# Performance work log

Measured on AMD Instinct MI355X. Metric: run time of the kernel, lower is better.

The kernel has to match this reference:

```python
import jax, jax.numpy as jnp
import numpy as np
import math

CH = 256
HW = 64
B = 4

def setup_inputs() -> dict:
    key = jax.random.key(0)
    ks = jax.random.split(key, 9)
    shp = (B, CH, HW, HW)
    return {
        "query": jax.random.normal(ks[0], shp, dtype=jnp.float32),
        "key":   jax.random.normal(ks[1], shp, dtype=jnp.float32),
        "value": jax.random.normal(ks[2], shp, dtype=jnp.float32),
        "wq": jax.random.normal(ks[3], (CH, CH), dtype=jnp.float32) * (1.0 / math.sqrt(CH)),
        "bq": jax.random.normal(ks[4], (CH,), dtype=jnp.float32) * 0.01,
        "wk": jax.random.normal(ks[5], (CH, CH), dtype=jnp.float32) * (1.0 / math.sqrt(CH)),
        "bk": jax.random.normal(ks[6], (CH,), dtype=jnp.float32) * 0.01,
        "wv": jax.random.normal(ks[7], (CH, CH), dtype=jnp.float32) * (1.0 / math.sqrt(CH)),
        "bv": jax.random.normal(ks[8], (CH,), dtype=jnp.float32) * 0.01,
    }

def _proj_to_tokens(x, w, b):
    # 1x1 conv == channel GEMM; output as (B, N, C) token layout
    Bz, C, H, W = x.shape
    # 'bchw,dc->bhwd' fuses the conv and the permute(0,2,1) after view
    t = jnp.einsum('bchw,dc->bhwd', x, w) + b  # (B,H,W,C)
    return t.reshape(Bz, H * W, C)

def reference(query, key, value, wq, bq, wk, bk, wv, bv):
    Bz, C, H, W = query.shape
    scale = 1.0 / jnp.sqrt(jnp.asarray(C, dtype=query.dtype))
    q = _proj_to_tokens(query, wq, bq)   # (B,N,C)
    k = _proj_to_tokens(key, wk, bk)     # (B,N,C)
    v = _proj_to_tokens(value, wv, bv)   # (B,N,C)
    attn = jnp.einsum('bnc,bmc->bnm', q, k) * scale  # (B,N,N)
    attn = jax.nn.softmax(attn, axis=-1)
    out = jnp.einsum('bnm,bmc->bnc', attn, v)        # (B,N,C)
    # permute back to (B,C,H,W)
    return out.transpose(0, 2, 1).reshape(Bz, C, H, W)
```

## Files before the change

### kernel.cpp

```cpp
#include <hip/hip_runtime.h>

typedef __attribute__((ext_vector_type(8))) short bf16x8;
typedef __attribute__((ext_vector_type(4))) float f32x4;
typedef __attribute__((ext_vector_type(4))) unsigned int u32x4;
typedef __attribute__((ext_vector_type(2))) unsigned int u32x2;

#define NTOK 4096
#define CHD 256
#define QSCALE 0.09016844005556022f
#define KB 32
#define NIT 32
#define RESCALE_THR 8.0f

typedef unsigned int __attribute__((address_space(1))) gu32;
typedef unsigned int __attribute__((address_space(3))) lu32;
#define GLOAD(g, s) __builtin_amdgcn_global_load_lds((const gu32*)(const void*)(g), (lu32*)(void*)(s), 16, 0, 0)

__device__ __forceinline__ unsigned short f2bf(float x) {
    unsigned int u = __builtin_bit_cast(unsigned int, x);
    return (unsigned short)((u + 0x7FFFu + ((u >> 16) & 1u)) >> 16);
}
__device__ __forceinline__ float bf2f(unsigned short u) {
    return __builtin_bit_cast(float, (unsigned int)u << 16);
}
__device__ __forceinline__ f32x4 mfma16(bf16x8 a, bf16x8 b, f32x4 c) {
    return __builtin_amdgcn_mfma_f32_16x16x32_bf16(a, b, c, 0, 0, 0);
}
__device__ __forceinline__ float xmax32(float x) {
    x = fmaxf(x, __shfl_xor(x, 16));
    x = fmaxf(x, __shfl_xor(x, 32));
    return x;
}
__device__ __forceinline__ float xsum32(float x) {
    x += __shfl_xor(x, 16);
    x += __shfl_xor(x, 32);
    return x;
}
__device__ __forceinline__ unsigned int cvtpk(float lo, float hi) {
    unsigned int r;
    asm("v_cvt_pk_bf16_f32 %0, %1, %2" : "=v"(r) : "v"(lo), "v"(hi));
    return r;
}

__global__ __launch_bounds__(256) void wconv_kernel(
    const float* __restrict__ wq, const float* __restrict__ wk,
    const float* __restrict__ wv, unsigned short* __restrict__ wbf)
{
    int idx = blockIdx.x * 256 + threadIdx.x;
    int z = idx >> 16;
    const float* src = (z == 0) ? wq : (z == 1) ? wk : wv;
    float s = (z == 0) ? QSCALE : 1.0f;
    wbf[idx] = f2bf(src[idx & 65535] * s);
}

__global__ __launch_bounds__(256) void proj_kernel(
    const float* __restrict__ xq, const float* __restrict__ xk, const float* __restrict__ xv,
    const float* __restrict__ bq, const float* __restrict__ bk, const float* __restrict__ bv,
    const unsigned short* __restrict__ wbf,
    unsigned short* __restrict__ Qo, unsigned short* __restrict__ Ko,
    unsigned short* __restrict__ VTo)
{
    __shared__ __align__(16) unsigned short alds[64 * 264];
    __shared__ __align__(16) unsigned char wlds[16384];
    const int z = blockIdx.y;
    const int b = blockIdx.x >> 6;
    const int n0 = (blockIdx.x & 63) << 6;
    const float* x    = (z == 0) ? xq : (z == 1) ? xk : xv;
    const float* bias = (z == 0) ? bq : (z == 1) ? bk : bv;
    const unsigned short* w = wbf + z * 65536;
    const int t = threadIdx.x;
    const int wv_ = t >> 6, l = t & 63, lr = l & 15, lg = l >> 4;

    #pragma unroll
    for (int it = 0; it < 16; ++it) {
        int idx = it * 256 + t;
        int c = idx >> 4, j4 = idx & 15;
        f32x4 v = *(const f32x4*)(x + (size_t)(b * CHD + c) * NTOK + n0 + j4 * 4);
        #pragma unroll
        for (int i = 0; i < 4; ++i)
            alds[(j4 * 4 + i) * 264 + c] = f2bf(v[i]);
    }
    __syncthreads();

    bf16x8 af[8];
    #pragma unroll
    for (int kk = 0; kk < 8; ++kk)
        af[kk] = *(const bf16x8*)&alds[(wv_ * 16 + lr) * 264 + kk * 32 + lg * 8];

    const float bsc = (z == 0) ? QSCALE : 1.0f;

    for (int dg = 0; dg < 8; ++dg) {
        __syncthreads();
        #pragma unroll
        for (int it = 0; it < 4; ++it) {
            int idx = it * 256 + t;
            int dr = idx >> 5, c16 = idx & 31;
            u32x4 vv = *(const u32x4*)(w + (size_t)(dg * 32 + dr) * CHD + c16 * 8);
            *(u32x4*)(wlds + ((dr * 512 + c16 * 16) ^ ((dr & 7) << 4))) = vv;
        }
        __syncthreads();
        #pragma unroll
        for (int dbi = 0; dbi < 2; ++dbi) {
            int dr = dbi * 16 + lr;
            int d = dg * 32 + dr;
            float bias_v = bias[d] * bsc;
            f32x4 acc = {bias_v, bias_v, bias_v, bias_v};
            #pragma unroll
            for (int kk = 0; kk < 8; ++kk) {
                bf16x8 bf = *(const bf16x8*)(wlds + ((dr * 512 + kk * 64 + lg * 16) ^ ((dr & 7) << 4)));
                acc = mfma16(af[kk], bf, acc);
            }
            if (z < 2) {
                unsigned short* o = (z == 0) ? Qo : Ko;
                #pragma unroll
                for (int r = 0; r < 4; ++r) {
                    int n = n0 + wv_ * 16 + lg * 4 + r;
                    o[(size_t)(b * NTOK + n) * CHD + d] = f2bf(acc[r]);
                }
            } else {
                int n = n0 + wv_ * 16 + lg * 4;
                u32x2 pk;
                pk[0] = (unsigned)f2bf(acc[0]) | ((unsigned)f2bf(acc[1]) << 16);
                pk[1] = (unsigned)f2bf(acc[2]) | ((unsigned)f2bf(acc[3]) << 16);
                *(u32x2*)(VTo + (size_t)(b * CHD + d) * NTOK + n) = pk;
            }
        }
    }
}

__global__ __attribute__((amdgpu_waves_per_eu(2, 2))) __launch_bounds__(512)
void attn_kernel(
    const unsigned short* __restrict__ Qp,
    const unsigned short* __restrict__ Kp,
    const unsigned short* __restrict__ VTp,
    unsigned short* __restrict__ Opart,
    float* __restrict__ Mpart, float* __restrict__ Lpart)
{
    __shared__ __align__(16) char smem[65536];
    const int bid = blockIdx.x;
    const int g = bid & 7, b = g >> 1, hf = g & 1;
    const int j = bid >> 3;
    const int q2 = j >> 4;
    const int n0 = (j & 15) * 256;
    const int part = hf * 2 + q2;
    const int kvbase = hf * 2048 + q2 * 1024;
    const int t = threadIdx.x;
    const int w = t >> 6, l = t & 63, lr = l & 15, lg = l >> 4;

    const char* Kby = (const char*)(Kp + (size_t)b * NTOK * CHD);
    const char* Vby = (const char*)(VTp + (size_t)b * CHD * NTOK);
    const unsigned short* Qb = Qp + (size_t)b * NTOK * CHD;

    bf16x8 qf[2][8];
    #pragma unroll
    for (int nb = 0; nb < 2; ++nb)
        #pragma unroll
        for (int kk = 0; kk < 8; ++kk)
            qf[nb][kk] = *(const bf16x8*)(Qb + (size_t)(n0 + w * 32 + nb * 16 + lr) * CHD + kk * 32 + lg * 8);
    asm volatile("" ::: "memory");

    auto stage = [&](int bsel, int kt2) {
        const char* ks = Kby + (size_t)(kvbase + kt2 * KB) * 512;
        const char* vs = Vby + (size_t)(kvbase + kt2 * KB) * 2;
        char* kd = smem + bsel * 32768 + w * 2048;
        char* vd = smem + bsel * 32768 + 16384 + w * 2048;
        #pragma unroll
        for (int jj = 0; jj < 2; ++jj) {
            int p = w * 2048 + jj * 1024 + l * 16;
            int i = p >> 9, c = p & 511;
            int pi = ((i >> 2) & 3) * 8 + ((i >> 4) & 1) * 4 + (i & 3);
            GLOAD(ks + pi * 512 + (c ^ ((i & 7) << 4)), kd + jj * 1024);
        }
        #pragma unroll
        for (int jj = 0; jj < 2; ++jj) {
            int p = w * 2048 + jj * 1024 + l * 16;
            GLOAD(vs + (p >> 6) * 8192 + (p & 63), vd + jj * 1024);
        }
    };

    stage(0, 0);

    f32x4 o[2][16];
    #pragma unroll
    for (int nb = 0; nb < 2; ++nb)
        #pragma unroll
        for (int db = 0; db < 16; ++db)
            o[nb][db] = (f32x4){0.f, 0.f, 0.f, 0.f};
    float mrow[2] = {-1e30f, -1e30f};
    float lpart[2] = {0.f, 0.f};

    #pragma unroll 1
    for (int kt = 0; kt < NIT; ++kt) {
        const int cur = kt & 1;
        asm volatile("s_waitcnt lgkmcnt(0) vmcnt(0)" ::: "memory");
        __builtin_amdgcn_s_barrier();
        __builtin_amdgcn_sched_barrier(0);
        if (kt + 1 < NIT) stage(cur ^ 1, kt + 1);

        const char* kB = smem + cur * 32768;
        const char* vB = kB + 16384;

        f32x4 s[2][2];
        #pragma unroll
        for (int nb = 0; nb < 2; ++nb)
            #pragma unroll
            for (int cb = 0; cb < 2; ++cb)
                s[nb][cb] = (f32x4){0.f, 0.f, 0.f, 0.f};
        __builtin_amdgcn_s_setprio(1);
        #pragma unroll
        for (int kk = 0; kk < 8; ++kk) {
            #pragma unroll
            for (int cb = 0; cb < 2; ++cb) {
                int row = cb * 16 + lr;
                bf16x8 kf = *(const bf16x8*)(kB + row * 512 + ((kk * 64 + lg * 16) ^ ((row & 7) << 4)));
                s[0][cb] = mfma16(kf, qf[0][kk], s[0][cb]);
                s[1][cb] = mfma16(kf, qf[1][kk], s[1][cb]);
            }
        }
        __builtin_amdgcn_s_setprio(0);

        float pm[2];
        #pragma unroll
        for (int nb = 0; nb < 2; ++nb) {
            float t8 = fmaxf(fmaxf(fmaxf(s[nb][0][0], s[nb][0][1]), fmaxf(s[nb][0][2], s[nb][0][3])),
                             fmaxf(fmaxf(s[nb][1][0], s[nb][1][1]), fmaxf(s[nb][1][2], s[nb][1][3])));
            pm[nb] = xmax32(t8);
        }
        bool grow = (pm[0] > mrow[0] + RESCALE_THR) || (pm[1] > mrow[1] + RESCALE_THR);
        if (__any((int)grow)) {
            #pragma unroll
            for (int nb = 0; nb < 2; ++nb) {
                float mn = fmaxf(mrow[nb], pm[nb]);
                float resc = __builtin_amdgcn_exp2f(mrow[nb] - mn);
                mrow[nb] = mn;
                lpart[nb] *= resc;
                f32x4 r4;
                #pragma unroll
                for (int r = 0; r < 4; ++r)
                    r4[r] = __shfl(resc, lg * 4 + r);
                #pragma unroll
                for (int db = 0; db < 16; ++db)
                    o[nb][db] *= r4;
            }
        }
        bf16x8 pb[2];
        #pragma unroll
        for (int nb = 0; nb < 2; ++nb) {
            float ps = 0.f;
            #pragma unroll
            for (int cb = 0; cb < 2; ++cb)
                #pragma unroll
                for (int r = 0; r < 4; ++r) {
                    float p = __builtin_amdgcn_exp2f(s[nb][cb][r] - mrow[nb]);
                    s[nb][cb][r] = p;
                    ps += p;
                }
            lpart[nb] += ps;
            u32x4 pw;
            pw[0] = cvtpk(s[nb][0][0], s[nb][0][1]);
            pw[1] = cvtpk(s[nb][0][2], s[nb][0][3]);
            pw[2] = cvtpk(s[nb][1][0], s[nb][1][1]);
            pw[3] = cvtpk(s[nb][1][2], s[nb][1][3]);
            pb[nb] = __builtin_bit_cast(bf16x8, pw);
        }

        __builtin_amdgcn_s_setprio(1);
        #pragma unroll
        for (int db = 0; db < 16; ++db) {
            bf16x8 vf = *(const bf16x8*)(vB + (db * 16 + lr) * 64 + lg * 16);
            o[0][db] = mfma16(pb[0], vf, o[0][db]);
            o[1][db] = mfma16(pb[1], vf, o[1][db]);
        }
        __builtin_amdgcn_s_setprio(0);
    }

    float lrow[2];
    #pragma unroll
    for (int nb = 0; nb < 2; ++nb)
        lrow[nb] = xsum32(lpart[nb]);

    unsigned short* Ob = Opart + (size_t)(b * 4 + part) * CHD * NTOK;
    #pragma unroll
    for (int nb = 0; nb < 2; ++nb)
        #pragma unroll
        for (int db = 0; db < 16; ++db) {
            int d = db * 16 + lr;
            int n = n0 + w * 32 + nb * 16 + lg * 4;
            u32x2 pk;
            pk[0] = (unsigned)f2bf(o[nb][db][0]) | ((unsigned)f2bf(o[nb][db][1]) << 16);
            pk[1] = (unsigned)f2bf(o[nb][db][2]) | ((unsigned)f2bf(o[nb][db][3]) << 16);
            *(u32x2*)(Ob + (size_t)d * NTOK + n) = pk;
        }
    if (lg == 0) {
        #pragma unroll
        for (int nb = 0; nb < 2; ++nb) {
            int n = n0 + w * 32 + nb * 16 + lr;
            Mpart[(size_t)(b * 4 + part) * NTOK + n] = mrow[nb];
            Lpart[(size_t)(b * 4 + part) * NTOK + n] = lrow[nb];
        }
    }
}

__global__ __launch_bounds__(256) void merge_kernel(
    const unsigned short* __restrict__ Opart,
    const float* __restrict__ Mpart, const float* __restrict__ Lpart,
    float* __restrict__ out)
{
    int tid = blockIdx.x * 256 + threadIdx.x;
    int n = (tid & 1023) * 4;
    int c = (tid >> 10) & 255;
    int b = tid >> 18;
    u32x2 ov[4]; f32x4 mv[4], lv[4];
    #pragma unroll
    for (int p = 0; p < 4; ++p) {
        ov[p] = *(const u32x2*)(Opart + (size_t)(b * 4 + p) * CHD * NTOK + (size_t)c * NTOK + n);
        mv[p] = *(const f32x4*)(Mpart + (size_t)(b * 4 + p) * NTOK + n);
        lv[p] = *(const f32x4*)(Lpart + (size_t)(b * 4 + p) * NTOK + n);
    }
    f32x4 res;
    #pragma unroll
    for (int r = 0; r < 4; ++r) {
        float mm = fmaxf(fmaxf(mv[0][r], mv[1][r]), fmaxf(mv[2][r], mv[3][r]));
        float num = 0.f, den = 0.f;
        #pragma unroll
        for (int p = 0; p < 4; ++p) {
            float sc = __builtin_amdgcn_exp2f(mv[p][r] - mm);
            num += bf2f((unsigned short)(ov[p][r >> 1] >> ((r & 1) * 16))) * sc;
            den += lv[p][r] * sc;
        }
        res[r] = num / den;
    }
    *(f32x4*)(out + (size_t)b * CHD * NTOK + (size_t)c * NTOK + n) = res;
}

extern "C" void kernel_launch(void* const* d_in, const int* in_sizes, int n_in,
                              void* d_out, int out_size, void* d_ws, size_t ws_size,
                              hipStream_t stream) {
    const float* xq = (const float*)d_in[0];
    const float* xk = (const float*)d_in[1];
    const float* xv = (const float*)d_in[2];
    const float* wq = (const float*)d_in[3];
    const float* bq = (const float*)d_in[4];
    const float* wk = (const float*)d_in[5];
    const float* bk = (const float*)d_in[6];
    const float* wv = (const float*)d_in[7];
    const float* bv = (const float*)d_in[8];

    char* ws = (char*)d_ws;
    unsigned short* wbf = (unsigned short*)ws;
    unsigned short* Qp  = (unsigned short*)(ws + 393216);
    unsigned short* Kp  = (unsigned short*)(ws + 8781824);
    unsigned short* VTp = (unsigned short*)(ws + 17170432);
    unsigned short* Op  = (unsigned short*)(ws + 25559040);
    float* Mp = (float*)(ws + 59113472);
    float* Lp = (float*)(ws + 59375616);

    hipLaunchKernelGGL(wconv_kernel, dim3(768), dim3(256), 0, stream, wq, wk, wv, wbf);
    hipLaunchKernelGGL(proj_kernel, dim3(256, 3), dim3(256), 0, stream,
                       xq, xk, xv, bq, bk, bv, wbf, Qp, Kp, VTp);
    hipLaunchKernelGGL(attn_kernel, dim3(256), dim3(512), 0, stream, Qp, Kp, VTp, Op, Mp, Lp);
    hipLaunchKernelGGL(merge_kernel, dim3(4096), dim3(256), 0, stream, Op, Mp, Lp, (float*)d_out);
}
```

Measured before the change: 126.2 us.

## Software-pipeline attention loop with 4-stage KV buffers and next-tile QK overlap

Raises LDS from 64KB to 128KB so K and V tiles sit in a 4-deep ring buffer, prefetched three tiles ahead. The loop is restructured so the QK^T MFMAs for tile kt+1 are issued alongside the PV MFMAs for tile kt, letting the softmax of the current tile overlap with matrix work. The aim is to hide global-load latency and the softmax bubbles between the two GEMMs. In exchange it doubles LDS use, which may limit occupancy (waves_per_eu is 2), adds the snext registers, and relies on precise vmcnt accounting to stay correct.

```diff
diff --git a/kernel.cpp b/kernel.cpp
--- a/kernel.cpp
+++ b/kernel.cpp
@@ -136,7 +136,7 @@
     unsigned short* __restrict__ Opart,
     float* __restrict__ Mpart, float* __restrict__ Lpart)
 {
-    __shared__ __align__(16) char smem[65536];
+    __shared__ __align__(16) char smem[131072];
     const int bid = blockIdx.x;
     const int g = bid & 7, b = g >> 1, hf = g & 1;
     const int j = bid >> 3;
@@ -159,11 +159,11 @@
             qf[nb][kk] = *(const bf16x8*)(Qb + (size_t)(n0 + w * 32 + nb * 16 + lr) * CHD + kk * 32 + lg * 8);
     asm volatile("" ::: "memory");
 
-    auto stage = [&](int bsel, int kt2) {
-        const char* ks = Kby + (size_t)(kvbase + kt2 * KB) * 512;
-        const char* vs = Vby + (size_t)(kvbase + kt2 * KB) * 2;
-        char* kd = smem + bsel * 32768 + w * 2048;
-        char* vd = smem + bsel * 32768 + 16384 + w * 2048;
+    auto stageKV = [&](int jt) {
+        const char* ks = Kby + (size_t)(kvbase + jt * KB) * 512;
+        const char* vs = Vby + (size_t)(kvbase + jt * KB) * 2;
+        char* kd = smem + (jt & 3) * 16384 + w * 2048;
+        char* vd = smem + 65536 + (jt & 3) * 16384 + w * 2048;
         #pragma unroll
         for (int jj = 0; jj < 2; ++jj) {
             int p = w * 2048 + jj * 1024 + l * 16;
@@ -178,35 +178,12 @@
         }
     };
 
-    stage(0, 0);
-
-    f32x4 o[2][16];
-    #pragma unroll
-    for (int nb = 0; nb < 2; ++nb)
-        #pragma unroll
-        for (int db = 0; db < 16; ++db)
-            o[nb][db] = (f32x4){0.f, 0.f, 0.f, 0.f};
-    float mrow[2] = {-1e30f, -1e30f};
-    float lpart[2] = {0.f, 0.f};
-
-    #pragma unroll 1
-    for (int kt = 0; kt < NIT; ++kt) {
-        const int cur = kt & 1;
-        asm volatile("s_waitcnt lgkmcnt(0) vmcnt(0)" ::: "memory");
-        __builtin_amdgcn_s_barrier();
-        __builtin_amdgcn_sched_barrier(0);
-        if (kt + 1 < NIT) stage(cur ^ 1, kt + 1);
-
-        const char* kB = smem + cur * 32768;
-        const char* vB = kB + 16384;
-
-        f32x4 s[2][2];
+    auto qkcompute = [&](const char* kB, f32x4 (&s)[2][2]) {
         #pragma unroll
         for (int nb = 0; nb < 2; ++nb)
             #pragma unroll
             for (int cb = 0; cb < 2; ++cb)
                 s[nb][cb] = (f32x4){0.f, 0.f, 0.f, 0.f};
-        __builtin_amdgcn_s_setprio(1);
         #pragma unroll
         for (int kk = 0; kk < 8; ++kk) {
             #pragma unroll
@@ -217,13 +194,31 @@
                 s[1][cb] = mfma16(kf, qf[1][kk], s[1][cb]);
             }
         }
-        __builtin_amdgcn_s_setprio(0);
-
+    };
+
+    stageKV(0); stageKV(1); stageKV(2);
+    asm volatile("s_waitcnt vmcnt(8)" ::: "memory");
+    __builtin_amdgcn_s_barrier();
+
+    f32x4 o[2][16];
+    #pragma unroll
+    for (int nb = 0; nb < 2; ++nb)
+        #pragma unroll
+        for (int db = 0; db < 16; ++db)
+            o[nb][db] = (f32x4){0.f, 0.f, 0.f, 0.f};
+    float mrow[2] = {-1e30f, -1e30f};
+    float lpart[2] = {0.f, 0.f};
+
+    f32x4 scur[2][2];
+    qkcompute(smem, scur);
+
+    #pragma unroll 1
+    for (int kt = 0; kt < NIT; ++kt) {
         float pm[2];
         #pragma unroll
         for (int nb = 0; nb < 2; ++nb) {
-            float t8 = fmaxf(fmaxf(fmaxf(s[nb][0][0], s[nb][0][1]), fmaxf(s[nb][0][2], s[nb][0][3])),
-                             fmaxf(fmaxf(s[nb][1][0], s[nb][1][1]), fmaxf(s[nb][1][2], s[nb][1][3])));
+            float t8 = fmaxf(fmaxf(fmaxf(scur[nb][0][0], scur[nb][0][1]), fmaxf(scur[nb][0][2], scur[nb][0][3])),
+                             fmaxf(fmaxf(scur[nb][1][0], scur[nb][1][1]), fmaxf(scur[nb][1][2], scur[nb][1][3])));
             pm[nb] = xmax32(t8);
         }
         bool grow = (pm[0] > mrow[0] + RESCALE_THR) || (pm[1] > mrow[1] + RESCALE_THR);
@@ -251,20 +246,37 @@
             for (int cb = 0; cb < 2; ++cb)
                 #pragma unroll
                 for (int r = 0; r < 4; ++r) {
-                    float p = __builtin_amdgcn_exp2f(s[nb][cb][r] - mrow[nb]);
-                    s[nb][cb][r] = p;
+                    float p = __builtin_amdgcn_exp2f(scur[nb][cb][r] - mrow[nb]);
+                    scur[nb][cb][r] = p;
                     ps += p;
                 }
             lpart[nb] += ps;
             u32x4 pw;
-            pw[0] = cvtpk(s[nb][0][0], s[nb][0][1]);
-            pw[1] = cvtpk(s[nb][0][2], s[nb][0][3]);
-            pw[2] = cvtpk(s[nb][1][0], s[nb][1][1]);
-            pw[3] = cvtpk(s[nb][1][2], s[nb][1][3]);
+            pw[0] = cvtpk(scur[nb][0][0], scur[nb][0][1]);
+            pw[1] = cvtpk(scur[nb][0][2], scur[nb][0][3]);
+            pw[2] = cvtpk(scur[nb][1][0], scur[nb][1][1]);
+            pw[3] = cvtpk(scur[nb][1][2], scur[nb][1][3]);
             pb[nb] = __builtin_bit_cast(bf16x8, pw);
         }
 
+        if (kt < NIT - 2) asm volatile("s_waitcnt lgkmcnt(0) vmcnt(4)" ::: "memory");
+        else              asm volatile("s_waitcnt lgkmcnt(0) vmcnt(0)" ::: "memory");
+        __builtin_amdgcn_s_barrier();
+        __builtin_amdgcn_sched_barrier(0);
+        if (kt + 3 < NIT) stageKV(kt + 3);
+
         __builtin_amdgcn_s_setprio(1);
+        f32x4 snext[2][2];
+        if (kt + 1 < NIT)
+            qkcompute(smem + ((kt + 1) & 3) * 16384, snext);
+        else {
+            #pragma unroll
+            for (int nb = 0; nb < 2; ++nb)
+                #pragma unroll
+                for (int cb = 0; cb < 2; ++cb)
+                    snext[nb][cb] = (f32x4){0.f, 0.f, 0.f, 0.f};
+        }
+        const char* vB = smem + 65536 + (kt & 3) * 16384;
         #pragma unroll
         for (int db = 0; db < 16; ++db) {
             bf16x8 vf = *(const bf16x8*)(vB + (db * 16 + lr) * 64 + lg * 16);
@@ -272,6 +284,12 @@
             o[1][db] = mfma16(pb[1], vf, o[1][db]);
         }
         __builtin_amdgcn_s_setprio(0);
+
+        #pragma unroll
+        for (int nb = 0; nb < 2; ++nb)
+            #pragma unroll
+            for (int cb = 0; cb < 2; ++cb)
+                scur[nb][cb] = snext[nb][cb];
     }
 
     float lrow[2];
```

Measured after the change: 163.8 us. 29.8% more time.
